# Kernel optimization log

Measured on AMD Instinct MI355X. Metric: run time of the kernel, lower is better.

## Reference

```python
import jax, jax.numpy as jnp
import numpy as np

DIM = 512
NUM_HEADS = 16
RANK = 4
HEAD_DIM = DIM // NUM_HEADS
SCALE = HEAD_DIM ** -0.5
B_, N, NW = 2048, 49, 64


def setup_inputs() -> dict:
    key = jax.random.key(0)
    ks = jax.random.split(key, 9)
    x = jax.random.normal(ks[0], (B_, N, DIM), dtype=jnp.float32)
    mask = jax.random.normal(ks[1], (NW, N, N), dtype=jnp.float32)
    # qkv base linear (torch Linear stores weight [out,in])
    W_qkv = jax.random.normal(ks[2], (3 * DIM, DIM), dtype=jnp.float32) * (DIM ** -0.5)
    b_qkv = jax.random.normal(ks[3], (3 * DIM,), dtype=jnp.float32) * 0.02
    # LoRA down [rank, dim], up [3*dim, rank] (zero-init in module; use small random for non-trivial math)
    A_down = jax.random.normal(ks[4], (RANK, DIM), dtype=jnp.float32) * 0.02
    B_up = jax.random.normal(ks[5], (3 * DIM, RANK), dtype=jnp.float32) * 0.02
    W_proj = jax.random.normal(ks[6], (DIM, DIM), dtype=jnp.float32) * (DIM ** -0.5)
    b_proj = jax.random.normal(ks[7], (DIM,), dtype=jnp.float32) * 0.02
    return {"x": x, "mask": mask, "W_qkv": W_qkv, "b_qkv": b_qkv,
            "A_down": A_down, "B_up": B_up, "W_proj": W_proj, "b_proj": b_proj}


def reference(x, mask, W_qkv, b_qkv, A_down, B_up, W_proj, b_proj):
    Bw, n, C = x.shape
    H, hd = NUM_HEADS, HEAD_DIM
    # LoRA-augmented QKV projection: base linear + up(down(x))
    qkv = x @ W_qkv.T + b_qkv + (x @ A_down.T) @ B_up.T          # [B_, N, 3C]
    qkv = qkv.reshape(Bw, n, 3, H, hd)
    q = qkv[:, :, 0].transpose(0, 2, 1, 3)                        # [B_, H, N, hd]
    k = qkv[:, :, 1].transpose(0, 2, 1, 3)
    v = qkv[:, :, 2].transpose(0, 2, 1, 3)
    attn = jnp.einsum('bhnd,bhmd->bhnm', q, k) * SCALE            # [B_, H, N, N]
    nW = mask.shape[0]
    attn = attn.reshape(Bw // nW, nW, H, n, n) + mask[None, :, None]
    attn = attn.reshape(Bw, H, n, n)
    attn = jax.nn.softmax(attn, axis=-1)
    out = jnp.einsum('bhnm,bhmd->bhnd', attn, v)                  # [B_, H, N, hd]
    out = out.transpose(0, 2, 1, 3).reshape(Bw, n, C)
    return out @ W_proj.T + b_proj
```

## Files before the change

kernel.cpp:

```cpp
#include <hip/hip_runtime.h>
#include <stdint.h>

typedef __attribute__((ext_vector_type(4))) float f32x4;
typedef __attribute__((ext_vector_type(8))) __bf16 bf16x8;
typedef __attribute__((ext_vector_type(4))) unsigned int u32x4;
typedef __attribute__((ext_vector_type(4))) unsigned short u16x4;

#define TOK 49
#define NHEAD 16
#define HDIM 32
#define CDIM 512
#define NB 2048
#define MTOT (NB * TOK)
#define ATT_SCALE 0.17677669529663687f

__device__ __forceinline__ unsigned short f2bf(float f) {
  uint32_t u = __builtin_bit_cast(uint32_t, f);
  u += 0x7FFFu + ((u >> 16) & 1u);
  return (unsigned short)(u >> 16);
}

__device__ __forceinline__ void gl_lds16(const void* g, const void* lds) {
  __builtin_amdgcn_global_load_lds(
      (__attribute__((address_space(1))) void*)(uintptr_t)g,
      (__attribute__((address_space(3))) void*)(uint32_t)(uintptr_t)lds,
      16, 0, 0);
}

__device__ __forceinline__ f32x4 mfma16(bf16x8 a, bf16x8 b, f32x4 c) {
  return __builtin_amdgcn_mfma_f32_16x16x32_bf16(a, b, c, 0, 0, 0);
}

__global__ __launch_bounds__(256) void k_prep_weff(
    const float* __restrict__ Wqkv, const float* __restrict__ Bup,
    const float* __restrict__ Adown, unsigned short* __restrict__ weff) {
  int idx = blockIdx.x * 256 + threadIdx.x;
  if (idx >= 3 * CDIM * CDIM) return;
  int o = idx >> 9, i = idx & 511;
  float v = Wqkv[idx];
#pragma unroll
  for (int r = 0; r < 4; r++) v += Bup[o * 4 + r] * Adown[r * 512 + i];
  weff[idx] = f2bf(v);
}

__global__ __launch_bounds__(256) void k_conv4(
    const float* __restrict__ src, unsigned short* __restrict__ dst, int n4) {
  for (int i = blockIdx.x * blockDim.x + threadIdx.x; i < n4;
       i += gridDim.x * blockDim.x) {
    f32x4 v = *(const f32x4*)(src + (size_t)i * 4);
    u16x4 o;
    o[0] = f2bf(v[0]); o[1] = f2bf(v[1]); o[2] = f2bf(v[2]); o[3] = f2bf(v[3]);
    *(u16x4*)(dst + (size_t)i * 4) = o;
  }
}

__global__ __launch_bounds__(512, 1) void k_gemm256qkv(
    const unsigned short* __restrict__ A, const unsigned short* __restrict__ Bw,
    const float* __restrict__ bias,
    unsigned short* __restrict__ qo, unsigned short* __restrict__ ko,
    unsigned short* __restrict__ vo) {
  __shared__ __attribute__((aligned(16))) unsigned short smem[65536];
  const int t = threadIdx.x;
  const int l = t & 63;
  const int l15 = l & 15, lq = l >> 4;
  const int w = t >> 6;
  const int wr = w >> 2, wc = w & 3;
  const int bid = blockIdx.x;
  const int lb = (bid & 7) * ((int)gridDim.x >> 3) + (bid >> 3);
  const int mt = lb / 6, nt = lb % 6;
  const size_t m0 = (size_t)mt * 256;
  const int n0 = nt * 256;

  auto stageA = [&](int kt, int bb) {
    unsigned short* dst = smem + bb * 16384;
#pragma unroll
    for (int q = 0; q < 4; ++q) {
      const int li = q * 512 + t;
      const int row = li >> 3, sl = li & 7;
      gl_lds16(A + (m0 + row) * CDIM + kt * 64 + ((sl ^ (row & 7)) << 3),
               &dst[li * 8]);
    }
  };
  auto stageB = [&](int kt, int bb) {
    unsigned short* dst = smem + 32768 + bb * 16384;
#pragma unroll
    for (int q = 0; q < 4; ++q) {
      const int li = q * 512 + t;
      const int row = li >> 3, sl = li & 7;
      gl_lds16(Bw + (size_t)(n0 + row) * CDIM + kt * 64 + ((sl ^ (row & 7)) << 3),
               &dst[li * 8]);
    }
  };

  f32x4 acc[8][4] = {};
  stageA(0, 0);
  stageB(0, 0);
  for (int kt = 0; kt < 8; ++kt) {
    const int cur = kt & 1, nb = cur ^ 1;
    if (kt < 7) {
      stageA(kt + 1, nb);
      stageB(kt + 1, nb);
      asm volatile("s_waitcnt vmcnt(8)" ::: "memory");
    } else {
      asm volatile("s_waitcnt vmcnt(0)" ::: "memory");
    }
    __builtin_amdgcn_s_barrier();
    asm volatile("" ::: "memory");
    const unsigned short* bufA = smem + cur * 16384;
    const unsigned short* bufB = smem + 32768 + cur * 16384;

    bf16x8 bfr[4][2];
#pragma unroll
    for (int c = 0; c < 4; ++c) {
      const int r = wc * 64 + c * 16 + l15;
#pragma unroll
      for (int h = 0; h < 2; ++h)
        bfr[c][h] = __builtin_bit_cast(
            bf16x8,
            *(const u32x4*)&bufB[r * 64 + (((lq + h * 4) ^ (r & 7)) << 3)]);
    }

#pragma unroll
    for (int p = 0; p < 4; ++p) {
      bf16x8 af[2][2];
#pragma unroll
      for (int rr = 0; rr < 2; ++rr) {
        const int r = wr * 128 + (p * 2 + rr) * 16 + l15;
#pragma unroll
        for (int h = 0; h < 2; ++h)
          af[rr][h] = __builtin_bit_cast(
              bf16x8,
              *(const u32x4*)&bufA[r * 64 + (((lq + h * 4) ^ (r & 7)) << 3)]);
      }
      __builtin_amdgcn_s_setprio(1);
#pragma unroll
      for (int rr = 0; rr < 2; ++rr) {
#pragma unroll
        for (int c = 0; c < 4; ++c) {
          acc[p * 2 + rr][c] = mfma16(af[rr][0], bfr[c][0], acc[p * 2 + rr][c]);
          acc[p * 2 + rr][c] = mfma16(af[rr][1], bfr[c][1], acc[p * 2 + rr][c]);
        }
      }
      __builtin_amdgcn_s_setprio(0);
    }
    asm volatile("" ::: "memory");
    __builtin_amdgcn_s_barrier();
  }

  __syncthreads();
  unsigned short* ep = smem + w * 8192;
#pragma unroll
  for (int J = 0; J < 4; ++J) {
    const int colb = n0 + wc * 64 + J * 16 + l15;
    const float bv = bias[colb];
    const int sl0 = J * 2 + (l15 >> 3);
#pragma unroll
    for (int I = 0; I < 8; ++I) {
#pragma unroll
      for (int r = 0; r < 4; ++r) {
        const int row = I * 16 + lq * 4 + r;
        ep[row * 64 + ((sl0 ^ (row & 7)) << 3) + (l15 & 7)] =
            f2bf(acc[I][J][r] + bv);
      }
    }
  }
  __syncthreads();
#pragma unroll
  for (int rnd = 0; rnd < 16; ++rnd) {
    const int sub = rnd * 16 + (l >> 2);
    const int mloc = sub >> 1, hd2 = sub & 1;
    const int colh = n0 + wc * 64 + hd2 * 32;
    const int which = colh >> 9;
    const int hh = (colh >> 5) & 15;
    unsigned short* dst = which == 0 ? qo : (which == 1 ? ko : vo);
    const uint32_t mg = (uint32_t)(m0 + wr * 128 + mloc);
    const uint32_t bw_ = mg / 49u;
    const uint32_t nn = mg - bw_ * 49u;
    const int sl = hd2 * 4 + (l & 3);
    u32x4 v = *(const u32x4*)&ep[mloc * 64 + ((sl ^ (mloc & 7)) << 3)];
    *(u32x4*)&dst[((size_t)(bw_ * 16u + hh) * 49u + nn) * 32u + (l & 3) * 8] = v;
  }
}

__global__ __launch_bounds__(256, 3) void k_gemm128(
    const unsigned short* __restrict__ A, const unsigned short* __restrict__ Bw,
    const float* __restrict__ bias, float* __restrict__ fo) {
  __shared__ __attribute__((aligned(16))) unsigned short smem[16384];
  const int t = threadIdx.x;
  const int l = t & 63;
  const int l15 = l & 15, lq = l >> 4;
  const int w = t >> 6;
  const int wr = w >> 1, wc = w & 1;
  const int bid = blockIdx.x;
  const int lb = (bid & 7) * ((int)gridDim.x >> 3) + (bid >> 3);
  const int mt = lb / 4, nt = lb % 4;
  const size_t m0 = (size_t)mt * 128;
  const int n0 = nt * 128;

  auto stageA = [&](int kt, int bb) {
    unsigned short* dst = smem + bb * 4096;
#pragma unroll
    for (int q = 0; q < 2; ++q) {
      const int li = q * 256 + t;
      const int row = li >> 2, sl = li & 3;
      gl_lds16(A + (m0 + row) * CDIM + kt * 32 + ((sl ^ ((row >> 1) & 3)) << 3),
               &dst[li * 8]);
    }
  };
  auto stageB = [&](int kt, int bb) {
    unsigned short* dst = smem + 8192 + bb * 4096;
#pragma unroll
    for (int q = 0; q < 2; ++q) {
      const int li = q * 256 + t;
      const int row = li >> 2, sl = li & 3;
      gl_lds16(Bw + (size_t)(n0 + row) * CDIM + kt * 32 +
                   ((sl ^ ((row >> 1) & 3)) << 3),
               &dst[li * 8]);
    }
  };

  f32x4 acc[4][4] = {};
  stageA(0, 0);
  stageB(0, 0);
  for (int kt = 0; kt < 16; ++kt) {
    const int cur = kt & 1, nb = cur ^ 1;
    if (kt < 15) {
      stageA(kt + 1, nb);
      stageB(kt + 1, nb);
      asm volatile("s_waitcnt vmcnt(4)" ::: "memory");
    } else {
      asm volatile("s_waitcnt vmcnt(0)" ::: "memory");
    }
    __builtin_amdgcn_s_barrier();
    asm volatile("" ::: "memory");
    const unsigned short* bufA = smem + cur * 4096;
    const unsigned short* bufB = smem + 8192 + cur * 4096;
    bf16x8 af[4], bfv[4];
#pragma unroll
    for (int f = 0; f < 4; ++f) {
      const int r = wr * 64 + f * 16 + l15;
      af[f] = __builtin_bit_cast(
          bf16x8, *(const u32x4*)&bufA[r * 32 + ((lq ^ ((r >> 1) & 3)) << 3)]);
    }
#pragma unroll
    for (int c = 0; c < 4; ++c) {
      const int r = wc * 64 + c * 16 + l15;
      bfv[c] = __builtin_bit_cast(
          bf16x8, *(const u32x4*)&bufB[r * 32 + ((lq ^ ((r >> 1) & 3)) << 3)]);
    }
    __builtin_amdgcn_s_setprio(1);
#pragma unroll
    for (int f = 0; f < 4; ++f) {
#pragma unroll
      for (int c = 0; c < 4; ++c) acc[f][c] = mfma16(af[f], bfv[c], acc[f][c]);
    }
    __builtin_amdgcn_s_setprio(0);
    asm volatile("" ::: "memory");
    __builtin_amdgcn_s_barrier();
  }

  __syncthreads();
  float* ep32 = (float*)smem + w * 2048;
#pragma unroll
  for (int ch = 0; ch < 2; ++ch) {
#pragma unroll
    for (int J = 0; J < 4; ++J) {
      const int colb = n0 + wc * 64 + J * 16 + l15;
      const float bv = bias[colb];
      const int sl0 = J * 4 + (l15 >> 2);
#pragma unroll
      for (int Ii = 0; Ii < 2; ++Ii) {
#pragma unroll
        for (int r = 0; r < 4; ++r) {
          const int row = Ii * 16 + lq * 4 + r;
          ep32[row * 64 + ((sl0 ^ (row & 7)) << 2) + (l15 & 3)] =
              acc[ch * 2 + Ii][J][r] + bv;
        }
      }
    }
    asm volatile("s_waitcnt lgkmcnt(0)" ::: "memory");
#pragma unroll
    for (int rnd = 0; rnd < 8; ++rnd) {
      const int row = rnd * 4 + (l >> 4);
      const int sl = l & 15;
      f32x4 v = *(const f32x4*)&ep32[row * 64 + ((sl ^ (row & 7)) << 2)];
      const size_t mg = m0 + wr * 64 + ch * 32 + row;
      *(f32x4*)&fo[mg * CDIM + n0 + wc * 64 + (l & 15) * 4] = v;
    }
    asm volatile("s_waitcnt lgkmcnt(0)" ::: "memory");
    asm volatile("" ::: "memory");
  }
}

__global__ __launch_bounds__(256) void k_attn(
    const unsigned short* __restrict__ qb, const unsigned short* __restrict__ kb,
    const unsigned short* __restrict__ vb, const float* __restrict__ mask,
    unsigned short* __restrict__ ao) {
  __shared__ __attribute__((aligned(16))) unsigned short sP[4][64 * 64];
  __shared__ __attribute__((aligned(16))) unsigned short sV[4][32 * 64];
  const int t = threadIdx.x;
  const int l = t & 63, w = t >> 6;
  const int l15 = l & 15, lq = l >> 4;
  const int pair = blockIdx.x * 4 + w;
  const int b = pair >> 4, h = pair & 15;
  const size_t base = (size_t)pair * (TOK * HDIM);
  unsigned short* P = sP[w];
  unsigned short* Vt = sV[w];

  bf16x8 qf[4], kf[4];
#pragma unroll
  for (int i = 0; i < 4; i++)
    qf[i] = __builtin_bit_cast(
        bf16x8, *(const u32x4*)(qb + base + (size_t)(i * 16 + l15) * 32 + lq * 8));
#pragma unroll
  for (int i = 0; i < 4; i++)
    kf[i] = __builtin_bit_cast(
        bf16x8, *(const u32x4*)(kb + base + (size_t)(i * 16 + l15) * 32 + lq * 8));
  u32x4 vr[4];
#pragma unroll
  for (int j = 0; j < 4; j++)
    vr[j] = *(const u32x4*)(vb + base + (size_t)l * 32 + j * 8);

  f32x4 s[4][4];
  __builtin_amdgcn_s_setprio(1);
#pragma unroll
  for (int i = 0; i < 4; i++) {
#pragma unroll
    for (int j = 0; j < 4; j++) s[i][j] = mfma16(qf[i], kf[j], (f32x4)0.0f);
  }
  __builtin_amdgcn_s_setprio(0);

  const bool vok = (l < TOK);
  const int tsl = ((l >> 3) & 7);
  const int tlo = l & 7;
#pragma unroll
  for (int j = 0; j < 4; j++) {
#pragma unroll
    for (int c = 0; c < 4; c++) {
      uint32_t u = vr[j][c];
      int d0 = j * 8 + c * 2;
      Vt[(d0 + 0) * 64 + ((tsl ^ ((d0 + 0) & 7)) << 3) + tlo] =
          vok ? (unsigned short)(u & 0xFFFFu) : (unsigned short)0;
      Vt[(d0 + 1) * 64 + ((tsl ^ ((d0 + 1) & 7)) << 3) + tlo] =
          vok ? (unsigned short)(u >> 16) : (unsigned short)0;
    }
  }

  const float* mrow = mask + (size_t)(b & 63) * (TOK * TOK);
#pragma unroll
  for (int i = 0; i < 4; i++) {
#pragma unroll
    for (int r = 0; r < 4; r++) {
      int row = i * 16 + lq * 4 + r;
#pragma unroll
      for (int j = 0; j < 4; j++) {
        int col = j * 16 + l15;
        float xv = s[i][j][r] * ATT_SCALE;
        if (col < TOK) {
          if (row < TOK) xv += mrow[row * TOK + col];
        } else {
          xv = -1e30f;
        }
        s[i][j][r] = xv;
      }
    }
  }

  float rinv[4][4];
#pragma unroll
  for (int i = 0; i < 4; i++) {
#pragma unroll
    for (int r = 0; r < 4; r++) {
      float m = fmaxf(fmaxf(s[i][0][r], s[i][1][r]), fmaxf(s[i][2][r], s[i][3][r]));
      m = fmaxf(m, __shfl_xor(m, 1));
      m = fmaxf(m, __shfl_xor(m, 2));
      m = fmaxf(m, __shfl_xor(m, 4));
      m = fmaxf(m, __shfl_xor(m, 8));
      float sum = 0.f;
      int row = i * 16 + lq * 4 + r;
#pragma unroll
      for (int j = 0; j < 4; j++) {
        float p = __expf(s[i][j][r] - m);
        sum += p;
        P[row * 64 + (((j * 2 + (l15 >> 3)) ^ (row & 7)) << 3) + (l15 & 7)] =
            f2bf(p);
      }
      sum += __shfl_xor(sum, 1);
      sum += __shfl_xor(sum, 2);
      sum += __shfl_xor(sum, 4);
      sum += __shfl_xor(sum, 8);
      rinv[i][r] = 1.0f / sum;
    }
  }

  asm volatile("s_waitcnt lgkmcnt(0)" ::: "memory");
  __builtin_amdgcn_sched_barrier(0);

  f32x4 o[4][2] = {};
#pragma unroll
  for (int ks = 0; ks < 2; ks++) {
    bf16x8 pa[4], vf[2];
#pragma unroll
    for (int i = 0; i < 4; i++)
      pa[i] = __builtin_bit_cast(
          bf16x8,
          *(const u32x4*)&P[(i * 16 + l15) * 64 + (((lq + ks * 4) ^ (l15 & 7)) << 3)]);
#pragma unroll
    for (int j = 0; j < 2; j++)
      vf[j] = __builtin_bit_cast(
          bf16x8,
          *(const u32x4*)&Vt[(j * 16 + l15) * 64 + (((lq + ks * 4) ^ (l15 & 7)) << 3)]);
    __builtin_amdgcn_s_setprio(1);
#pragma unroll
    for (int i = 0; i < 4; i++) {
#pragma unroll
      for (int j = 0; j < 2; j++) o[i][j] = mfma16(pa[i], vf[j], o[i][j]);
    }
    __builtin_amdgcn_s_setprio(0);
  }

#pragma unroll
  for (int i = 0; i < 4; i++) {
#pragma unroll
    for (int r = 0; r < 4; r++) {
      int row = i * 16 + lq * 4 + r;
      if (row < TOK) {
        float inv = rinv[i][r];
        size_t obase = ((size_t)b * TOK + row) * CDIM + h * HDIM;
#pragma unroll
        for (int j = 0; j < 2; j++)
          ao[obase + j * 16 + l15] = f2bf(o[i][j][r] * inv);
      }
    }
  }
}

extern "C" void kernel_launch(void* const* d_in, const int* in_sizes, int n_in,
                              void* d_out, int out_size, void* d_ws,
                              size_t ws_size, hipStream_t stream) {
  const float* x = (const float*)d_in[0];
  const float* mask = (const float*)d_in[1];
  const float* Wqkv = (const float*)d_in[2];
  const float* bqkv = (const float*)d_in[3];
  const float* Adown = (const float*)d_in[4];
  const float* Bup = (const float*)d_in[5];
  const float* Wproj = (const float*)d_in[6];
  const float* bproj = (const float*)d_in[7];
  float* out = (float*)d_out;
  char* ws = (char*)d_ws;

  size_t off = 0;
  auto alloc = [&](size_t bytes) {
    size_t o = off;
    off += (bytes + 255) & ~(size_t)255;
    return o;
  };
  const size_t qkv_elems = (size_t)NB * NHEAD * TOK * HDIM;
  unsigned short* weff = (unsigned short*)(ws + alloc((size_t)3 * CDIM * CDIM * 2));
  unsigned short* wpb = (unsigned short*)(ws + alloc((size_t)CDIM * CDIM * 2));
  unsigned short* qb = (unsigned short*)(ws + alloc(qkv_elems * 2 + 4096));
  unsigned short* kb = (unsigned short*)(ws + alloc(qkv_elems * 2 + 4096));
  unsigned short* vb = (unsigned short*)(ws + alloc(qkv_elems * 2 + 4096));
  unsigned short* xb = (unsigned short*)(ws + alloc((size_t)MTOT * CDIM * 2));
  unsigned short* ao = xb;

  k_prep_weff<<<(3 * CDIM * CDIM + 255) / 256, 256, 0, stream>>>(Wqkv, Bup,
                                                                 Adown, weff);
  k_conv4<<<256, 256, 0, stream>>>(Wproj, wpb, CDIM * CDIM / 4);
  k_conv4<<<2048, 256, 0, stream>>>(x, xb, MTOT * CDIM / 4);
  k_gemm256qkv<<<(MTOT / 256) * 6, 512, 0, stream>>>(xb, weff, bqkv, qb, kb, vb);
  k_attn<<<NB * NHEAD / 4, 256, 0, stream>>>(qb, kb, vb, mask, ao);
  k_gemm128<<<(MTOT / 128) * 4, 256, 0, stream>>>(ao, wpb, bproj, out);
}
```

Baseline: 561.4 us.

## Switch QKV and proj GEMMs to triple-buffered LDS pipeline with one barrier

Both GEMM kernels move from a double-buffered K loop with two barriers per step to a three-stage ring buffer. Each step issues the load for step kt+2 after the barrier, so the trailing barrier can be dropped. The QKV GEMM also drops its K tile from 64 to 32 to fit three stages in less LDS. Its epilogue now runs in two halves to fit the smaller shared buffer. This aims to hide global-load latency and cut barrier stalls, but it doubles the loop iteration count for the QKV kernel and adds extra barriers in the epilogue.

```diff
diff --git a/kernel.cpp b/kernel.cpp
--- a/kernel.cpp
+++ b/kernel.cpp
@@ -59,7 +59,7 @@
     const float* __restrict__ bias,
     unsigned short* __restrict__ qo, unsigned short* __restrict__ ko,
     unsigned short* __restrict__ vo) {
-  __shared__ __attribute__((aligned(16))) unsigned short smem[65536];
+  __shared__ __attribute__((aligned(16))) unsigned short smem[49152];
   const int t = threadIdx.x;
   const int l = t & 63;
   const int l15 = l & 15, lq = l >> 4;
@@ -71,121 +71,107 @@
   const size_t m0 = (size_t)mt * 256;
   const int n0 = nt * 256;
 
-  auto stageA = [&](int kt, int bb) {
-    unsigned short* dst = smem + bb * 16384;
-#pragma unroll
-    for (int q = 0; q < 4; ++q) {
+  auto stage = [&](int kt, int bb) {
+    unsigned short* dA = smem + bb * 8192;
+    unsigned short* dB = smem + 24576 + bb * 8192;
+#pragma unroll
+    for (int q = 0; q < 2; ++q) {
       const int li = q * 512 + t;
-      const int row = li >> 3, sl = li & 7;
-      gl_lds16(A + (m0 + row) * CDIM + kt * 64 + ((sl ^ (row & 7)) << 3),
-               &dst[li * 8]);
+      const int row = li >> 2, sl = li & 3;
+      const int kof = kt * 32 + ((sl ^ ((row >> 1) & 3)) << 3);
+      gl_lds16(A + (m0 + row) * CDIM + kof, &dA[li * 8]);
+    }
+#pragma unroll
+    for (int q = 0; q < 2; ++q) {
+      const int li = q * 512 + t;
+      const int row = li >> 2, sl = li & 3;
+      const int kof = kt * 32 + ((sl ^ ((row >> 1) & 3)) << 3);
+      gl_lds16(Bw + (size_t)(n0 + row) * CDIM + kof, &dB[li * 8]);
     }
   };
-  auto stageB = [&](int kt, int bb) {
-    unsigned short* dst = smem + 32768 + bb * 16384;
-#pragma unroll
-    for (int q = 0; q < 4; ++q) {
-      const int li = q * 512 + t;
-      const int row = li >> 3, sl = li & 7;
-      gl_lds16(Bw + (size_t)(n0 + row) * CDIM + kt * 64 + ((sl ^ (row & 7)) << 3),
-               &dst[li * 8]);
-    }
-  };
 
   f32x4 acc[8][4] = {};
-  stageA(0, 0);
-  stageB(0, 0);
-  for (int kt = 0; kt < 8; ++kt) {
-    const int cur = kt & 1, nb = cur ^ 1;
-    if (kt < 7) {
-      stageA(kt + 1, nb);
-      stageB(kt + 1, nb);
-      asm volatile("s_waitcnt vmcnt(8)" ::: "memory");
+  stage(0, 0);
+  stage(1, 1);
+  for (int kt = 0; kt < 16; ++kt) {
+    const int cur = kt % 3;
+    if (kt < 15) {
+      asm volatile("s_waitcnt vmcnt(4)" ::: "memory");
     } else {
       asm volatile("s_waitcnt vmcnt(0)" ::: "memory");
     }
     __builtin_amdgcn_s_barrier();
     asm volatile("" ::: "memory");
-    const unsigned short* bufA = smem + cur * 16384;
-    const unsigned short* bufB = smem + 32768 + cur * 16384;
-
-    bf16x8 bfr[4][2];
+    if (kt < 14) stage(kt + 2, (kt + 2) % 3);
+    const unsigned short* bufA = smem + cur * 8192;
+    const unsigned short* bufB = smem + 24576 + cur * 8192;
+    bf16x8 bfv[4], af[8];
 #pragma unroll
     for (int c = 0; c < 4; ++c) {
       const int r = wc * 64 + c * 16 + l15;
-#pragma unroll
-      for (int h = 0; h < 2; ++h)
-        bfr[c][h] = __builtin_bit_cast(
-            bf16x8,
-            *(const u32x4*)&bufB[r * 64 + (((lq + h * 4) ^ (r & 7)) << 3)]);
-    }
-
-#pragma unroll
-    for (int p = 0; p < 4; ++p) {
-      bf16x8 af[2][2];
-#pragma unroll
-      for (int rr = 0; rr < 2; ++rr) {
-        const int r = wr * 128 + (p * 2 + rr) * 16 + l15;
-#pragma unroll
-        for (int h = 0; h < 2; ++h)
-          af[rr][h] = __builtin_bit_cast(
-              bf16x8,
-              *(const u32x4*)&bufA[r * 64 + (((lq + h * 4) ^ (r & 7)) << 3)]);
-      }
-      __builtin_amdgcn_s_setprio(1);
-#pragma unroll
-      for (int rr = 0; rr < 2; ++rr) {
-#pragma unroll
-        for (int c = 0; c < 4; ++c) {
-          acc[p * 2 + rr][c] = mfma16(af[rr][0], bfr[c][0], acc[p * 2 + rr][c]);
-          acc[p * 2 + rr][c] = mfma16(af[rr][1], bfr[c][1], acc[p * 2 + rr][c]);
+      bfv[c] = __builtin_bit_cast(
+          bf16x8, *(const u32x4*)&bufB[r * 32 + ((lq ^ ((r >> 1) & 3)) << 3)]);
+    }
+#pragma unroll
+    for (int f = 0; f < 8; ++f) {
+      const int r = wr * 128 + f * 16 + l15;
+      af[f] = __builtin_bit_cast(
+          bf16x8, *(const u32x4*)&bufA[r * 32 + ((lq ^ ((r >> 1) & 3)) << 3)]);
+    }
+    __builtin_amdgcn_s_setprio(1);
+#pragma unroll
+    for (int f = 0; f < 8; ++f) {
+#pragma unroll
+      for (int c = 0; c < 4; ++c) acc[f][c] = mfma16(af[f], bfv[c], acc[f][c]);
+    }
+    __builtin_amdgcn_s_setprio(0);
+    asm volatile("" ::: "memory");
+  }
+
+  __syncthreads();
+  unsigned short* ep = smem + w * 4096;
+#pragma unroll
+  for (int half = 0; half < 2; ++half) {
+#pragma unroll
+    for (int J = 0; J < 4; ++J) {
+      const int colb = n0 + wc * 64 + J * 16 + l15;
+      const float bv = bias[colb];
+      const int sl0 = J * 2 + (l15 >> 3);
+#pragma unroll
+      for (int I = 0; I < 4; ++I) {
+#pragma unroll
+        for (int r = 0; r < 4; ++r) {
+          const int row = I * 16 + lq * 4 + r;
+          ep[row * 64 + ((sl0 ^ (row & 7)) << 3) + (l15 & 7)] =
+              f2bf(acc[half * 4 + I][J][r] + bv);
         }
       }
-      __builtin_amdgcn_s_setprio(0);
-    }
-    asm volatile("" ::: "memory");
-    __builtin_amdgcn_s_barrier();
-  }
-
-  __syncthreads();
-  unsigned short* ep = smem + w * 8192;
-#pragma unroll
-  for (int J = 0; J < 4; ++J) {
-    const int colb = n0 + wc * 64 + J * 16 + l15;
-    const float bv = bias[colb];
-    const int sl0 = J * 2 + (l15 >> 3);
-#pragma unroll
-    for (int I = 0; I < 8; ++I) {
-#pragma unroll
-      for (int r = 0; r < 4; ++r) {
-        const int row = I * 16 + lq * 4 + r;
-        ep[row * 64 + ((sl0 ^ (row & 7)) << 3) + (l15 & 7)] =
-            f2bf(acc[I][J][r] + bv);
-      }
-    }
-  }
-  __syncthreads();
-#pragma unroll
-  for (int rnd = 0; rnd < 16; ++rnd) {
-    const int sub = rnd * 16 + (l >> 2);
-    const int mloc = sub >> 1, hd2 = sub & 1;
-    const int colh = n0 + wc * 64 + hd2 * 32;
-    const int which = colh >> 9;
-    const int hh = (colh >> 5) & 15;
-    unsigned short* dst = which == 0 ? qo : (which == 1 ? ko : vo);
-    const uint32_t mg = (uint32_t)(m0 + wr * 128 + mloc);
-    const uint32_t bw_ = mg / 49u;
-    const uint32_t nn = mg - bw_ * 49u;
-    const int sl = hd2 * 4 + (l & 3);
-    u32x4 v = *(const u32x4*)&ep[mloc * 64 + ((sl ^ (mloc & 7)) << 3)];
-    *(u32x4*)&dst[((size_t)(bw_ * 16u + hh) * 49u + nn) * 32u + (l & 3) * 8] = v;
+    }
+    __syncthreads();
+#pragma unroll
+    for (int rnd = 0; rnd < 8; ++rnd) {
+      const int sub = rnd * 16 + (l >> 2);
+      const int mloc = sub >> 1, hd2 = sub & 1;
+      const int colh = n0 + wc * 64 + hd2 * 32;
+      const int which = colh >> 9;
+      const int hh = (colh >> 5) & 15;
+      unsigned short* dst = which == 0 ? qo : (which == 1 ? ko : vo);
+      const uint32_t mg = (uint32_t)(m0 + wr * 128 + half * 64 + mloc);
+      const uint32_t bw_ = mg / 49u;
+      const uint32_t nn = mg - bw_ * 49u;
+      const int sl = hd2 * 4 + (l & 3);
+      u32x4 v = *(const u32x4*)&ep[mloc * 64 + ((sl ^ (mloc & 7)) << 3)];
+      *(u32x4*)&dst[((size_t)(bw_ * 16u + hh) * 49u + nn) * 32u + (l & 3) * 8] =
+          v;
+    }
+    __syncthreads();
   }
 }
 
 __global__ __launch_bounds__(256, 3) void k_gemm128(
     const unsigned short* __restrict__ A, const unsigned short* __restrict__ Bw,
     const float* __restrict__ bias, float* __restrict__ fo) {
-  __shared__ __attribute__((aligned(16))) unsigned short smem[16384];
+  __shared__ __attribute__((aligned(16))) unsigned short smem[24576];
   const int t = threadIdx.x;
   const int l = t & 63;
   const int l15 = l & 15, lq = l >> 4;
@@ -197,57 +183,53 @@
   const size_t m0 = (size_t)mt * 128;
   const int n0 = nt * 128;
 
-  auto stageA = [&](int kt, int bb) {
-    unsigned short* dst = smem + bb * 4096;
+  auto stage = [&](int kt, int bb) {
+    unsigned short* dA = smem + bb * 4096;
+    unsigned short* dB = smem + 12288 + bb * 4096;
 #pragma unroll
     for (int q = 0; q < 2; ++q) {
       const int li = q * 256 + t;
       const int row = li >> 2, sl = li & 3;
-      gl_lds16(A + (m0 + row) * CDIM + kt * 32 + ((sl ^ ((row >> 1) & 3)) << 3),
-               &dst[li * 8]);
-    }
-  };
-  auto stageB = [&](int kt, int bb) {
-    unsigned short* dst = smem + 8192 + bb * 4096;
+      const int kof = kt * 32 + ((sl ^ ((row >> 1) & 3)) << 3);
+      gl_lds16(A + (m0 + row) * CDIM + kof, &dA[li * 8]);
+    }
 #pragma unroll
     for (int q = 0; q < 2; ++q) {
       const int li = q * 256 + t;
       const int row = li >> 2, sl = li & 3;
-      gl_lds16(Bw + (size_t)(n0 + row) * CDIM + kt * 32 +
-                   ((sl ^ ((row >> 1) & 3)) << 3),
-               &dst[li * 8]);
+      const int kof = kt * 32 + ((sl ^ ((row >> 1) & 3)) << 3);
+      gl_lds16(Bw + (size_t)(n0 + row) * CDIM + kof, &dB[li * 8]);
     }
   };
 
   f32x4 acc[4][4] = {};
-  stageA(0, 0);
-  stageB(0, 0);
+  stage(0, 0);
+  stage(1, 1);
   for (int kt = 0; kt < 16; ++kt) {
-    const int cur = kt & 1, nb = cur ^ 1;
+    const int cur = kt % 3;
     if (kt < 15) {
-      stageA(kt + 1, nb);
-      stageB(kt + 1, nb);
       asm volatile("s_waitcnt vmcnt(4)" ::: "memory");
     } else {
       asm volatile("s_waitcnt vmcnt(0)" ::: "memory");
     }
     __builtin_amdgcn_s_barrier();
     asm volatile("" ::: "memory");
+    if (kt < 14) stage(kt + 2, (kt + 2) % 3);
     const unsigned short* bufA = smem + cur * 4096;
-    const unsigned short* bufB = smem + 8192 + cur * 4096;
+    const unsigned short* bufB = smem + 12288 + cur * 4096;
     bf16x8 af[4], bfv[4];
+#pragma unroll
+    for (int c = 0; c < 4; ++c) {
+      const int r = wc * 64 + c * 16 + l15;
+      bfv[c] = __builtin_bit_cast(
+          bf16x8, *(const u32x4*)&bufB[r * 32 + ((lq ^ ((r >> 1) & 3)) << 3)]);
+    }
 #pragma unroll
     for (int f = 0; f < 4; ++f) {
       const int r = wr * 64 + f * 16 + l15;
       af[f] = __builtin_bit_cast(
           bf16x8, *(const u32x4*)&bufA[r * 32 + ((lq ^ ((r >> 1) & 3)) << 3)]);
     }
-#pragma unroll
-    for (int c = 0; c < 4; ++c) {
-      const int r = wc * 64 + c * 16 + l15;
-      bfv[c] = __builtin_bit_cast(
-          bf16x8, *(const u32x4*)&bufB[r * 32 + ((lq ^ ((r >> 1) & 3)) << 3)]);
-    }
     __builtin_amdgcn_s_setprio(1);
 #pragma unroll
     for (int f = 0; f < 4; ++f) {
@@ -256,7 +238,6 @@
     }
     __builtin_amdgcn_s_setprio(0);
     asm volatile("" ::: "memory");
-    __builtin_amdgcn_s_barrier();
   }
 
   __syncthreads();
```

Result: no change. 559.3 us (-0.4%).
